# Optimization experiments

Measured on AMD Instinct MI355X. Metric: run time of the kernel, lower is better.

The kernel has to match this reference:

```python
import jax, jax.numpy as jnp
import numpy as np
from jax import lax

PI = 3.141592653589793

def _sobel_kernel(dtype):
    # (2,1,3,3): channel 0 = d/dx (Sobel x), channel 1 = d/dy (Sobel y)
    sx = jnp.array([[-1., 0., 1.], [-2., 0., 2.], [-1., 0., 1.]], dtype=dtype)
    sy = jnp.array([[-1., -2., -1.], [0., 0., 0.], [1., 2., 1.]], dtype=dtype)
    return jnp.stack([sx, sy], axis=0)[:, None]

def _orientation_weights(dtype):
    # angles pi/8, 3pi/8, ..., 15pi/8 -> rows (cos, sin); last 2 rows = identity (copy dx, dy)
    angles = (2.0 * jnp.arange(8, dtype=dtype) + 1.0) * (PI / 8.0)
    basis = jnp.stack([jnp.cos(angles), jnp.sin(angles)], axis=1)  # (8,2)
    return jnp.concatenate([basis, jnp.eye(2, dtype=dtype)], axis=0)  # (10,2)

def setup_inputs() -> dict:
    key = jax.random.key(0)
    x = jax.random.normal(key, (1, 1, 4096, 4096), dtype=jnp.float32)
    return {"x": x}

def reference(x):
    dt = x.dtype
    # 1) image gradients via Sobel conv, pad 1 -> (1,2,H,W)
    grads = lax.conv_general_dilated(
        x, _sobel_kernel(dt), window_strides=(1, 1), padding=[(1, 1), (1, 1)],
        dimension_numbers=("NCHW", "OIHW", "NCHW"))
    # 2) 1x1 orientation conv: (10,2) basis dot product -> (1,10,H,W)
    W = _orientation_weights(dt)
    feats = jnp.einsum("oc,bchw->bohw", W, grads)
    cosines = feats[:, :8]        # (1,8,H,W)
    dx, dy = feats[:, 8], feats[:, 9]
    # 3) histogram layer: one-hot argmax over orientation fibre, weighted by |grad|
    mag = jnp.sqrt(dx * dx + dy * dy)                      # (1,H,W)
    idx = jnp.argmax(cosines, axis=1)                      # (1,H,W) int
    occupancy = jax.nn.one_hot(idx, 8, axis=1, dtype=dt)   # (1,8,H,W)
    hist = occupancy * mag[:, None]                        # (1,8,H,W)
    # 4) subgrid accumulation: depthwise 4x4 ones conv, pad 2 -> (1,8,H+1,W+1)
    ones_k = jnp.ones((8, 1, 4, 4), dtype=dt)
    out = lax.conv_general_dilated(
        hist, ones_k, window_strides=(1, 1), padding=[(2, 2), (2, 2)],
        dimension_numbers=("NCHW", "OIHW", "NCHW"), feature_group_count=8)
    return out
```

## Files before the change

kernel.cpp:

```cpp
#include <hip/hip_runtime.h>
#include <math.h>

#define N   4096
#define NO  4097
#define TO  32
#define GW  129

struct OrientCoef { float c[8]; float s[8]; };

__global__ __launch_bounds__(256, 6) void sift_fused(const float* __restrict__ x,
                                                     float* __restrict__ out,
                                                     OrientCoef cf) {
    int bid = blockIdx.y * GW + blockIdx.x;
    {
        const int nwg = GW * GW;
        const int q = nwg / 8, r = nwg % 8;
        int xcd = bid & 7, local = bid >> 3;
        bid = (xcd < r ? xcd * (q + 1) : r * (q + 1) + (xcd - r) * q) + local;
    }
    const int i0  = (bid / GW) * TO;
    const int j0  = (bid % GW) * TO;
    const int tid = threadIdx.x;

    __shared__ float xs[37][38];
    __shared__ float packed[35][36];

    for (int l = tid; l < 37 * 37; l += 256) {
        int lr = l / 37, lc = l % 37;
        int gr = i0 - 3 + lr, gc = j0 - 3 + lc;
        float v = 0.0f;
        if (gr >= 0 && gr < N && gc >= 0 && gc < N) v = x[(size_t)gr * N + gc];
        xs[lr][lc] = v;
    }
    __syncthreads();

    for (int l = tid; l < 35 * 35; l += 256) {
        int lr = l / 35, lc = l % 35;
        int gr = i0 - 2 + lr, gc = j0 - 2 + lc;
        float pv = 0.0f;
        if (gr >= 0 && gr < N && gc >= 0 && gc < N) {
            float x00 = xs[lr][lc],     x01 = xs[lr][lc + 1],     x02 = xs[lr][lc + 2];
            float x10 = xs[lr + 1][lc],                           x12 = xs[lr + 1][lc + 2];
            float x20 = xs[lr + 2][lc], x21 = xs[lr + 2][lc + 1], x22 = xs[lr + 2][lc + 2];
            float dx = (x02 - x00) + 2.0f * (x12 - x10) + (x22 - x20);
            float dy = (x20 - x00) + 2.0f * (x21 - x01) + (x22 - x02);
            float mag = sqrtf(dx * dx + dy * dy);
            int best = 0;
            float bv = fmaf(cf.s[0], dy, cf.c[0] * dx);
            #pragma unroll
            for (int o = 1; o < 8; ++o) {
                float cs = fmaf(cf.s[o], dy, cf.c[o] * dx);
                if (cs > bv) { bv = cs; best = o; }
            }
            pv = __uint_as_float((__float_as_uint(mag) & ~7u) | (unsigned)best);
        }
        packed[lr][lc] = pv;
    }
    __syncthreads();

    {
        const int rg = tid >> 5;
        const int jt = tid & 31;
        const int j  = j0 + jt;
        const bool jok = (j < NO);
        const int rbase = rg * 4;

        float w0[8], w1[8], w2[8];
        #pragma unroll
        for (int rr = 0; rr < 7; ++rr) {
            const int r = rbase + rr;
            float m0 = packed[r][jt],     m1 = packed[r][jt + 1];
            float m2 = packed[r][jt + 2], m3 = packed[r][jt + 3];
            unsigned b0 = __float_as_uint(m0) & 7u, b1 = __float_as_uint(m1) & 7u;
            unsigned b2 = __float_as_uint(m2) & 7u, b3 = __float_as_uint(m3) & 7u;
            float h[8];
            #pragma unroll
            for (int o = 0; o < 8; ++o) {
                unsigned uo = (unsigned)o;
                float s = (b0 == uo) ? m0 : 0.0f;
                s += (b1 == uo) ? m1 : 0.0f;
                s += (b2 == uo) ? m2 : 0.0f;
                s += (b3 == uo) ? m3 : 0.0f;
                h[o] = s;
            }
            if (rr >= 3) {
                int i = i0 + rbase + rr - 3;
                if (jok && i < NO) {
                    #pragma unroll
                    for (int o = 0; o < 8; ++o)
                        out[((size_t)o * NO + i) * NO + j] =
                            (w0[o] + w1[o]) + (w2[o] + h[o]);
                }
            }
            #pragma unroll
            for (int o = 0; o < 8; ++o) { w0[o] = w1[o]; w1[o] = w2[o]; w2[o] = h[o]; }
        }
    }
}

extern "C" void kernel_launch(void* const* d_in, const int* in_sizes, int n_in,
                              void* d_out, int out_size, void* d_ws, size_t ws_size,
                              hipStream_t stream) {
    const float* x = (const float*)d_in[0];
    float* out = (float*)d_out;

    OrientCoef cf;
    const float pi8 = (float)(M_PI / 8.0);
    for (int o = 0; o < 8; ++o) {
        float angle = (float)(2 * o + 1) * pi8;
        cf.c[o] = (float)cos((double)angle);
        cf.s[o] = (float)sin((double)angle);
    }

    dim3 grid(GW, GW);
    sift_fused<<<grid, dim3(256), 0, stream>>>(x, out, cf);
}
```

Before: 657.1 us.

## Split tile into per-wavefront strips with wave barriers and vectorized Sobel

Each 64-lane wavefront now owns an 8-row strip of the 32x32 output tile and loads its own 13x37 halo into a private shared-memory slice. This replaces block-wide __syncthreads with wave barriers and lets waves skip out-of-range rows early. The Sobel/orientation stage has each lane compute four adjacent pixels from float4 LDS reads, which cuts LDS traffic. In exchange the vertical halo is loaded redundantly per wave, so more global reads are issued for the same output.

```diff
diff --git a/kernel.cpp b/kernel.cpp
--- a/kernel.cpp
+++ b/kernel.cpp
@@ -18,59 +18,83 @@
         int xcd = bid & 7, local = bid >> 3;
         bid = (xcd < r ? xcd * (q + 1) : r * (q + 1) + (xcd - r) * q) + local;
     }
-    const int i0  = (bid / GW) * TO;
-    const int j0  = (bid % GW) * TO;
-    const int tid = threadIdx.x;
+    const int i0   = (bid / GW) * TO;
+    const int j0   = (bid % GW) * TO;
+    const int tid  = threadIdx.x;
+    const int wv   = tid >> 6;
+    const int lane = tid & 63;
 
-    __shared__ float xs[37][38];
-    __shared__ float packed[35][36];
+    const int wi0 = i0 + wv * 8;
+    if (wi0 >= NO) return;
 
-    for (int l = tid; l < 37 * 37; l += 256) {
-        int lr = l / 37, lc = l % 37;
-        int gr = i0 - 3 + lr, gc = j0 - 3 + lc;
-        float v = 0.0f;
-        if (gr >= 0 && gr < N && gc >= 0 && gc < N) v = x[(size_t)gr * N + gc];
-        xs[lr][lc] = v;
+    __shared__ float xs[4][13][40];
+    __shared__ float pk[4][11][36];
+
+    #pragma unroll
+    for (int k = 0; k < 8; ++k) {
+        int l = lane + 64 * k;
+        if (l < 13 * 37) {
+            int lr = l / 37, lc = l - 37 * lr;
+            int gr = wi0 - 3 + lr, gc = j0 - 3 + lc;
+            float v = 0.0f;
+            if (gr >= 0 && gr < N && gc >= 0 && gc < N) v = x[(size_t)gr * N + gc];
+            xs[wv][lr][lc] = v;
+        }
     }
-    __syncthreads();
+    __builtin_amdgcn_wave_barrier();
 
-    for (int l = tid; l < 35 * 35; l += 256) {
-        int lr = l / 35, lc = l % 35;
-        int gr = i0 - 2 + lr, gc = j0 - 2 + lc;
-        float pv = 0.0f;
-        if (gr >= 0 && gr < N && gc >= 0 && gc < N) {
-            float x00 = xs[lr][lc],     x01 = xs[lr][lc + 1],     x02 = xs[lr][lc + 2];
-            float x10 = xs[lr + 1][lc],                           x12 = xs[lr + 1][lc + 2];
-            float x20 = xs[lr + 2][lc], x21 = xs[lr + 2][lc + 1], x22 = xs[lr + 2][lc + 2];
-            float dx = (x02 - x00) + 2.0f * (x12 - x10) + (x22 - x20);
-            float dy = (x20 - x00) + 2.0f * (x21 - x01) + (x22 - x02);
-            float mag = sqrtf(dx * dx + dy * dy);
-            int best = 0;
-            float bv = fmaf(cf.s[0], dy, cf.c[0] * dx);
+    #pragma unroll
+    for (int it = 0; it < 2; ++it) {
+        int u = lane + 64 * it;
+        if (u < 99) {
+            int r = u / 9, g = u - 9 * r;
+            int c0 = 4 * g;
+            const int  grc = wi0 - 2 + r;
+            const bool rok = (grc >= 0) && (grc < N);
+            float f0[8], f1[8], f2[8];
+            *(float4*)&f0[0] = *(const float4*)&xs[wv][r][c0];
+            *(float4*)&f0[4] = *(const float4*)&xs[wv][r][c0 + 4];
+            *(float4*)&f1[0] = *(const float4*)&xs[wv][r + 1][c0];
+            *(float4*)&f1[4] = *(const float4*)&xs[wv][r + 1][c0 + 4];
+            *(float4*)&f2[0] = *(const float4*)&xs[wv][r + 2][c0];
+            *(float4*)&f2[4] = *(const float4*)&xs[wv][r + 2][c0 + 4];
+            float pv[4];
             #pragma unroll
-            for (int o = 1; o < 8; ++o) {
-                float cs = fmaf(cf.s[o], dy, cf.c[o] * dx);
-                if (cs > bv) { bv = cs; best = o; }
+            for (int k = 0; k < 4; ++k) {
+                float dx = (f0[k+2] - f0[k]) + 2.0f * (f1[k+2] - f1[k]) + (f2[k+2] - f2[k]);
+                float dy = (f2[k] - f0[k]) + 2.0f * (f2[k+1] - f0[k+1]) + (f2[k+2] - f0[k+2]);
+                float mag = sqrtf(dx * dx + dy * dy);
+                int best = 0;
+                float bv = fmaf(cf.s[0], dy, cf.c[0] * dx);
+                #pragma unroll
+                for (int o = 1; o < 8; ++o) {
+                    float cs = fmaf(cf.s[o], dy, cf.c[o] * dx);
+                    if (cs > bv) { bv = cs; best = o; }
+                }
+                int gcc = j0 - 2 + c0 + k;
+                pv[k] = (rok && gcc >= 0 && gcc < N)
+                      ? __uint_as_float((__float_as_uint(mag) & ~7u) | (unsigned)best)
+                      : 0.0f;
             }
-            pv = __uint_as_float((__float_as_uint(mag) & ~7u) | (unsigned)best);
+            *(float4*)&pk[wv][r][c0] = *(const float4*)&pv[0];
         }
-        packed[lr][lc] = pv;
     }
-    __syncthreads();
+    __builtin_amdgcn_wave_barrier();
 
     {
-        const int rg = tid >> 5;
-        const int jt = tid & 31;
-        const int j  = j0 + jt;
+        const int rg  = lane >> 5;
+        const int jt  = lane & 31;
+        const int j   = j0 + jt;
         const bool jok = (j < NO);
-        const int rbase = rg * 4;
-
+        const size_t NO2 = (size_t)NO * NO;
         float w0[8], w1[8], w2[8];
         #pragma unroll
+        for (int o = 0; o < 8; ++o) { w0[o] = 0.f; w1[o] = 0.f; w2[o] = 0.f; }
+        #pragma unroll
         for (int rr = 0; rr < 7; ++rr) {
-            const int r = rbase + rr;
-            float m0 = packed[r][jt],     m1 = packed[r][jt + 1];
-            float m2 = packed[r][jt + 2], m3 = packed[r][jt + 3];
+            const int r = rg * 4 + rr;
+            float m0 = pk[wv][r][jt],     m1 = pk[wv][r][jt + 1];
+            float m2 = pk[wv][r][jt + 2], m3 = pk[wv][r][jt + 3];
             unsigned b0 = __float_as_uint(m0) & 7u, b1 = __float_as_uint(m1) & 7u;
             unsigned b2 = __float_as_uint(m2) & 7u, b3 = __float_as_uint(m3) & 7u;
             float h[8];
@@ -84,12 +108,12 @@
                 h[o] = s;
             }
             if (rr >= 3) {
-                int i = i0 + rbase + rr - 3;
+                int i = wi0 + rg * 4 + rr - 3;
                 if (jok && i < NO) {
+                    float* op = out + (size_t)i * NO + j;
                     #pragma unroll
                     for (int o = 0; o < 8; ++o)
-                        out[((size_t)o * NO + i) * NO + j] =
-                            (w0[o] + w1[o]) + (w2[o] + h[o]);
+                        op[(size_t)o * NO2] = (w0[o] + w1[o]) + (w2[o] + h[o]);
                 }
             }
             #pragma unroll
```

Result: no change. 666.7 us (+1.5%).
